# Kernel optimization log

Hardware: AMD Instinct MI355X
Metric: run time of the kernel (lower is better)

Reference implementation:

```python
import jax, jax.numpy as jnp
import numpy as np

N, IN, H0, H1 = 8192, 128, 512, 256
ITER = 10
EPS = 1e-5


def _bn(h, g, b):
    # BatchNorm1d in training mode: biased batch stats
    mu = h.mean(axis=0)
    var = h.var(axis=0)
    return g * (h - mu) * jax.lax.rsqrt(var + EPS) + b


def setup_inputs() -> dict:
    key = jax.random.key(0)
    ks = jax.random.split(key, 8)
    x = jax.random.normal(ks[0], (N, IN), dtype=jnp.float32)
    W = jax.random.uniform(ks[1], (N, N), dtype=jnp.float32)  # torch.rand
    W1 = jax.random.normal(ks[2], (H0, IN), dtype=jnp.float32) * (1.0 / np.sqrt(IN))
    b1 = jnp.zeros((H0,), jnp.float32)
    g1 = jnp.ones((H0,), jnp.float32)
    be1 = jnp.zeros((H0,), jnp.float32)
    W2 = jax.random.normal(ks[3], (H1, H0), dtype=jnp.float32) * (1.0 / np.sqrt(H0))
    b2 = jnp.zeros((H1,), jnp.float32)
    g2 = jnp.ones((H1,), jnp.float32)
    be2 = jnp.zeros((H1,), jnp.float32)
    fcw = jax.random.normal(ks[4], (1, H1), dtype=jnp.float32) * (1.0 / np.sqrt(H1))
    fcb = jnp.zeros((1,), jnp.float32)
    return {"x": x, "W": W, "W1": W1, "b1": b1, "g1": g1, "be1": be1,
            "W2": W2, "b2": b2, "g2": g2, "be2": be2, "fcw": fcw, "fcb": fcb}


def reference(x, W, W1, b1, g1, be1, W2, b2, g2, be2, fcw, fcb):
    h = jax.nn.leaky_relu(_bn(x @ W1.T + b1, g1, be1), 0.01)        # [N, H0]
    feats = jax.nn.leaky_relu(_bn(h @ W2.T + b2, g2, be2), 0.01)    # [N, H1]
    logits = feats @ fcw.T + fcb                                    # [N, 1]
    fn = jnp.linalg.norm(feats, axis=1, keepdims=True)              # [N, 1]
    pairwise_sim = (feats @ feats.T) / (fn @ fn.T)                  # [N, N]
    W_sym = (W + W.T) * 0.5
    PP = pairwise_sim * W_sym                                       # [N, N]
    unary = logits
    def body(i, lg):
        coef = 1.0 - 2.0 * jax.nn.sigmoid(lg)                       # (1-p) - p, [N,1]
        # E_i = sum_j (1-2 p_j) * PP[i, j]  -> matvec
        return unary + PP @ coef
    logits = jax.lax.fori_loop(0, ITER, body, logits)
    return logits
```

## Files before the change

kernel.cpp:

```cpp
#include <hip/hip_runtime.h>
#include <hip/hip_bf16.h>

#define NROWS 8192
#define NITER 10

typedef __attribute__((ext_vector_type(8))) short bf16x8;
typedef __attribute__((ext_vector_type(8))) unsigned short u16x8;
typedef __attribute__((ext_vector_type(16))) float f32x16;

__device__ __forceinline__ float bf2f(unsigned short u) {
  union { float f; unsigned int i; } c; c.i = ((unsigned int)u) << 16; return c.f;
}
__device__ __forceinline__ unsigned short f2bf(float f) {
  unsigned int x = __float_as_uint(f);
  unsigned int r = (x + 0x7FFFu + ((x >> 16) & 1u)) >> 16;
  return (unsigned short)r;
}

#define TRIS(b) ((b) * (257 - (b)) / 2)
__device__ __forceinline__ void tril_decode(int L, int& bi, int& bj) {
  int b = (int)((257.0f - sqrtf((float)(66049 - 8 * L))) * 0.5f);
  if (b > 127) b = 127;
  if (b < 0) b = 0;
  while (b < 127 && TRIS(b + 1) <= L) ++b;
  while (b > 0 && TRIS(b) > L) --b;
  bi = b;
  bj = b + (L - TRIS(b));
}

#define TRIS64(b) ((b) * (129 - (b)) / 2)
__device__ __forceinline__ void tril64_decode(int L, int& bi, int& bj) {
  int b = (int)((129.0f - sqrtf((float)(16641 - 8 * L))) * 0.5f);
  if (b > 63) b = 63;
  if (b < 0) b = 0;
  while (b < 63 && TRIS64(b + 1) <= L) ++b;
  while (b > 0 && TRIS64(b) > L) --b;
  bi = b;
  bj = b + (L - TRIS64(b));
}

__global__ __launch_bounds__(256) void cast3(const float* __restrict__ x,
                                             const float* __restrict__ W1,
                                             const float* __restrict__ W2,
                                             unsigned short* __restrict__ xb,
                                             unsigned short* __restrict__ w1b,
                                             unsigned short* __restrict__ w2b) {
  int idx = blockIdx.x * 256 + threadIdx.x;
  const float* src; unsigned short* dst; int l;
  if (idx < 131072) { src = x; dst = xb; l = idx; }
  else if (idx < 139264) { src = W1; dst = w1b; l = idx - 131072; }
  else if (idx < 155648) { src = W2; dst = w2b; l = idx - 139264; }
  else return;
  const float4* p = (const float4*)src + (size_t)l * 2;
  float4 a = p[0], b = p[1];
  u16x8 o;
  o[0] = f2bf(a.x); o[1] = f2bf(a.y); o[2] = f2bf(a.z); o[3] = f2bf(a.w);
  o[4] = f2bf(b.x); o[5] = f2bf(b.y); o[6] = f2bf(b.z); o[7] = f2bf(b.w);
  *(u16x8*)(dst + (size_t)l * 8) = o;
}

__global__ __launch_bounds__(256) void gemm_bt_mfma_stats(
    const unsigned short* __restrict__ A, const unsigned short* __restrict__ B,
    unsigned short* __restrict__ Cb, float* __restrict__ pS, float* __restrict__ pQ,
    int NN, int K) {
  __shared__ __align__(16) unsigned short Asw[4096];
  __shared__ __align__(16) unsigned short Bsw[4096];
  __shared__ float Sarr[4][64], Qarr[4][64];
  const int i0 = blockIdx.x * 64, j0 = blockIdx.y * 64;
  const int t = threadIdx.x;
  const int lane = t & 63;
  const int wv = t >> 6;
  const int wi = wv >> 1, wj = wv & 1;
  const int khalf = lane >> 5;

  f32x16 acc;
#pragma unroll
  for (int r = 0; r < 16; ++r) acc[r] = 0.f;

  const int lrow = t >> 2;
  const int lgp = (t & 3) * 2;
  const int arow = wi * 32 + (lane & 31);
  const int brow = wj * 32 + (lane & 31);
  const int nc = K >> 6;
#pragma unroll 1
  for (int c = 0; c < nc; ++c) {
    const unsigned short* sa = A + (size_t)(i0 + lrow) * K + c * 64 + lgp * 8;
    const unsigned short* sb = B + (size_t)(j0 + lrow) * K + c * 64 + lgp * 8;
    u16x8 va0 = *(const u16x8*)(sa);
    u16x8 va1 = *(const u16x8*)(sa + 8);
    u16x8 vb0 = *(const u16x8*)(sb);
    u16x8 vb1 = *(const u16x8*)(sb + 8);
    __syncthreads();
    int s0 = (lgp ^ (lrow & 7)) * 8;
    int s1 = ((lgp + 1) ^ (lrow & 7)) * 8;
    *(u16x8*)&Asw[lrow * 64 + s0] = va0;
    *(u16x8*)&Asw[lrow * 64 + s1] = va1;
    *(u16x8*)&Bsw[lrow * 64 + s0] = vb0;
    *(u16x8*)&Bsw[lrow * 64 + s1] = vb1;
    __syncthreads();
#pragma unroll
    for (int s = 0; s < 4; ++s) {
      int slot = s * 2 + khalf;
      bf16x8 a = *(const bf16x8*)&Asw[arow * 64 + ((slot ^ (arow & 7)) * 8)];
      bf16x8 b = *(const bf16x8*)&Bsw[brow * 64 + ((slot ^ (brow & 7)) * 8)];
      acc = __builtin_amdgcn_mfma_f32_32x32x16_bf16(a, b, acc, 0, 0, 0);
    }
  }
  float s = 0.f, q = 0.f;
#pragma unroll
  for (int r = 0; r < 16; ++r) {
    int rowl = (r & 3) + 8 * (r >> 2) + 4 * khalf;
    int coll = lane & 31;
    float v = acc[r];
    s += v; q += v * v;
    Cb[(size_t)(i0 + wi * 32 + rowl) * NN + j0 + wj * 32 + coll] = f2bf(v);
  }
  Sarr[wv][lane] = s;
  Qarr[wv][lane] = q;
  __syncthreads();
  if (t < 64) {
    int wjc = t >> 5, coll = t & 31;
    float st = (Sarr[wjc][coll] + Sarr[wjc][coll + 32]) +
               (Sarr[wjc + 2][coll] + Sarr[wjc + 2][coll + 32]);
    float qt = (Qarr[wjc][coll] + Qarr[wjc][coll + 32]) +
               (Qarr[wjc + 2][coll] + Qarr[wjc + 2][coll + 32]);
    pS[(size_t)blockIdx.x * NN + j0 + t] = st;
    pQ[(size_t)blockIdx.x * NN + j0 + t] = qt;
  }
}

__global__ void bn_finalize(const float* __restrict__ pS, const float* __restrict__ pQ,
                            const float* __restrict__ g, const float* __restrict__ be,
                            float2* __restrict__ ab, int C) {
  int c = blockIdx.x * 256 + threadIdx.x;
  if (c >= C) return;
  float s = 0.f, q = 0.f;
  for (int r = 0; r < 128; ++r) { s += pS[(size_t)r * C + c]; q += pQ[(size_t)r * C + c]; }
  const float invM = 1.f / 8192.f;
  float mu = s * invM;
  float var = q * invM - mu * mu;
  float rstd = rsqrtf(var + 1e-5f);
  float a = g[c] * rstd;
  ab[c] = make_float2(a, be[c] - mu * a);
}

__global__ __launch_bounds__(256) void bn_apply(const unsigned short* __restrict__ hraw,
                                                const float2* __restrict__ ab,
                                                unsigned short* __restrict__ hb,
                                                int Cmask) {
  size_t idx = (size_t)blockIdx.x * 256 + threadIdx.x;
  u16x8 v = *(const u16x8*)(hraw + idx * 8);
  int cb = (int)((idx * 8) & (size_t)Cmask);
  u16x8 o;
#pragma unroll
  for (int k = 0; k < 8; ++k) {
    float2 a = ab[cb + k];
    float r = a.x * bf2f(v[k]) + a.y;
    r = r >= 0.f ? r : 0.01f * r;
    o[k] = f2bf(r);
  }
  *(u16x8*)(hb + idx * 8) = o;
}

__global__ __launch_bounds__(256) void bn_rowfn(const unsigned short* __restrict__ fraw,
                                                const float2* __restrict__ ab,
                                                const float* __restrict__ fcw,
                                                const float* __restrict__ fcb,
                                                unsigned short* __restrict__ fnorm,
                                                float* __restrict__ unary,
                                                float* __restrict__ coef0) {
  const int lane = threadIdx.x & 63;
  const int row = blockIdx.x * 4 + (threadIdx.x >> 6);
  ushort4 v4 = *(const ushort4*)(fraw + (size_t)row * 256 + lane * 4);
  float4 w = *(const float4*)(fcw + lane * 4);
  int c = lane * 4;
  float2 a0 = ab[c], a1 = ab[c + 1], a2 = ab[c + 2], a3 = ab[c + 3];
  float f0 = a0.x * bf2f(v4.x) + a0.y; f0 = f0 >= 0.f ? f0 : 0.01f * f0;
  float f1 = a1.x * bf2f(v4.y) + a1.y; f1 = f1 >= 0.f ? f1 : 0.01f * f1;
  float f2 = a2.x * bf2f(v4.z) + a2.y; f2 = f2 >= 0.f ? f2 : 0.01f * f2;
  float f3 = a3.x * bf2f(v4.w) + a3.y; f3 = f3 >= 0.f ? f3 : 0.01f * f3;
  float ssq = f0 * f0 + f1 * f1 + f2 * f2 + f3 * f3;
  float dot = f0 * w.x + f1 * w.y + f2 * w.z + f3 * w.w;
#pragma unroll
  for (int o = 32; o; o >>= 1) { ssq += __shfl_xor(ssq, o); dot += __shfl_xor(dot, o); }
  float rfn = rsqrtf(ssq);
  *(ushort4*)(fnorm + (size_t)row * 256 + lane * 4) =
      make_ushort4(f2bf(f0 * rfn), f2bf(f1 * rfn), f2bf(f2 * rfn), f2bf(f3 * rfn));
  if (lane == 0) {
    float lg = dot + fcb[0];
    unary[row] = lg;
    coef0[row] = 1.f - 2.f / (1.f + __expf(-lg));
  }
}

__global__ __launch_bounds__(256) void ppbuild_sym(const unsigned short* __restrict__ fnorm,
                                                   const float* __restrict__ W,
                                                   unsigned short* __restrict__ PP) {
  int bi, bj;
  tril_decode(blockIdx.x, bi, bj);
  const int i0 = bi * 64, j0 = bj * 64;

  __shared__ __align__(16) unsigned char shm[18944];
  unsigned short* Asw = (unsigned short*)shm;
  unsigned short* Bsw = (unsigned short*)shm + 4736;
  float (*Wt)[68] = (float(*)[68])shm;
  unsigned short* OutD = (unsigned short*)shm;

  const int t = threadIdx.x;
  const int lane = t & 63;
  const int wv = t >> 6;
  const int wi = wv >> 1, wj = wv & 1;
  const int khalf = lane >> 5;

  f32x16 acc;
#pragma unroll
  for (int r = 0; r < 16; ++r) acc[r] = 0.f;

  const int lrow = t >> 2;
  const int lgp = (t & 3) * 2;
  const int arow = wi * 32 + (lane & 31);
  const int brow = wj * 32 + (lane & 31);
#pragma unroll 1
  for (int c = 0; c < 4; ++c) {
    const unsigned short* sa = fnorm + (size_t)(i0 + lrow) * 256 + c * 64 + lgp * 8;
    const unsigned short* sb = fnorm + (size_t)(j0 + lrow) * 256 + c * 64 + lgp * 8;
    u16x8 va0 = *(const u16x8*)(sa);
    u16x8 va1 = *(const u16x8*)(sa + 8);
    u16x8 vb0 = *(const u16x8*)(sb);
    u16x8 vb1 = *(const u16x8*)(sb + 8);
    __syncthreads();
    int s0 = (lgp ^ (lrow & 7)) * 8;
    int s1 = ((lgp + 1) ^ (lrow & 7)) * 8;
    *(u16x8*)&Asw[lrow * 64 + s0] = va0;
    *(u16x8*)&Asw[lrow * 64 + s1] = va1;
    *(u16x8*)&Bsw[lrow * 64 + s0] = vb0;
    *(u16x8*)&Bsw[lrow * 64 + s1] = vb1;
    __syncthreads();
#pragma unroll
    for (int s = 0; s < 4; ++s) {
      int slot = s * 2 + khalf;
      bf16x8 a = *(const bf16x8*)&Asw[arow * 64 + ((slot ^ (arow & 7)) * 8)];
      bf16x8 b = *(const bf16x8*)&Bsw[brow * 64 + ((slot ^ (brow & 7)) * 8)];
      acc = __builtin_amdgcn_mfma_f32_32x32x16_bf16(a, b, acc, 0, 0, 0);
    }
  }

  __syncthreads();
  {
    const int j = t >> 2, cb = (t & 3) * 16;
    const float* src = W + (size_t)(j0 + j) * NROWS + i0 + cb;
#pragma unroll
    for (int q = 0; q < 4; ++q) {
      float4 v = *(const float4*)(src + q * 4);
      Wt[j][cb + q * 4 + 0] = v.x; Wt[j][cb + q * 4 + 1] = v.y;
      Wt[j][cb + q * 4 + 2] = v.z; Wt[j][cb + q * 4 + 3] = v.w;
    }
  }
  __syncthreads();
  unsigned short pb[16];
#pragma unroll
  for (int r = 0; r < 16; ++r) {
    int rowl = (r & 3) + 8 * (r >> 2) + 4 * khalf;
    int coll = lane & 31;
    int il = wi * 32 + rowl, jl = wj * 32 + coll;
    float wd = W[(size_t)(i0 + il) * NROWS + (j0 + jl)];
    float ws = 0.5f * (wd + Wt[jl][il]);
    pb[r] = f2bf(acc[r] * ws);
  }
  __syncthreads();
#pragma unroll
  for (int r = 0; r < 16; ++r) {
    int rowl = (r & 3) + 8 * (r >> 2) + 4 * khalf;
    int coll = lane & 31;
    OutD[(wi * 32 + rowl) * 74 + wj * 32 + coll] = pb[r];
  }
  __syncthreads();
  const int row = t >> 3;
  const int seg = t & 7;
#pragma unroll
  for (int q = 0; q < 2; ++q) {
    int rr = row + q * 32;
    const unsigned int* pd = (const unsigned int*)(OutD + rr * 74 + seg * 8);
    union { u16x8 v; unsigned int u[4]; } dd;
#pragma unroll
    for (int k = 0; k < 4; ++k) dd.u[k] = pd[k];
    *(u16x8*)(PP + (size_t)(i0 + rr) * NROWS + j0 + seg * 8) = dd.v;
  }
}

__global__ __launch_bounds__(256) void ppmv_sym(const unsigned short* __restrict__ PP,
                                                const float* __restrict__ coef_in,
                                                float* __restrict__ pE) {
  int bi, bj;
  tril64_decode(blockIdx.x, bi, bj);
  const int i0 = bi * 128, j0 = bj * 128;
  const int t = threadIdx.x;

  __shared__ __align__(16) unsigned short tile[128][132];
  __shared__ float cj[128], ci[128];
  __shared__ float Tw[8][128];
  __shared__ float Dred[128];

  if (t < 128) cj[t] = coef_in[j0 + t];
  else ci[t - 128] = coef_in[i0 + (t - 128)];
  {
    const int r = t >> 1, h = (t & 1) * 64;
    const unsigned short* src = PP + (size_t)(i0 + r) * NROWS + j0 + h;
#pragma unroll
    for (int q = 0; q < 8; ++q)
      *(u16x8*)&tile[r][h + q * 8] = *(const u16x8*)(src + q * 8);
  }
  __syncthreads();
  {
    const int r = t >> 1, h = (t & 1) * 64;
    float a = 0.f;
#pragma unroll
    for (int q = 0; q < 8; ++q) {
      u16x8 v = *(const u16x8*)&tile[r][h + q * 8];
      float4 c0 = *(const float4*)&cj[h + q * 8];
      float4 c1 = *(const float4*)&cj[h + q * 8 + 4];
      a += bf2f(v[0]) * c0.x + bf2f(v[1]) * c0.y + bf2f(v[2]) * c0.z + bf2f(v[3]) * c0.w;
      a += bf2f(v[4]) * c1.x + bf2f(v[5]) * c1.y + bf2f(v[6]) * c1.z + bf2f(v[7]) * c1.w;
    }
    a += __shfl_xor(a, 1);
    if ((t & 1) == 0) Dred[r] = a;
  }
  {
    const int c4 = (t & 31) * 4, rg = t >> 5;
    float a0 = 0.f, a1 = 0.f, a2 = 0.f, a3 = 0.f;
#pragma unroll
    for (int k = 0; k < 16; ++k) {
      int row = rg * 16 + k;
      ushort4 v = *(const ushort4*)&tile[row][c4];
      float s = ci[row];
      a0 += bf2f(v.x) * s; a1 += bf2f(v.y) * s;
      a2 += bf2f(v.z) * s; a3 += bf2f(v.w) * s;
    }
    Tw[rg][c4] = a0; Tw[rg][c4 + 1] = a1;
    Tw[rg][c4 + 2] = a2; Tw[rg][c4 + 3] = a3;
  }
  __syncthreads();
  if (t < 128) {
    pE[(size_t)bj * NROWS + i0 + t] = Dred[t];
    if (bi != bj) {
      float s = ((Tw[0][t] + Tw[1][t]) + (Tw[2][t] + Tw[3][t])) +
                ((Tw[4][t] + Tw[5][t]) + (Tw[6][t] + Tw[7][t]));
      pE[(size_t)bi * NROWS + j0 + t] = s;
    }
  }
}

__global__ __launch_bounds__(256) void ppmv_reduce(const float* __restrict__ pE,
                                                   const float* __restrict__ unary,
                                                   float* __restrict__ coef_out,
                                                   float* __restrict__ lg_out) {
  int row = blockIdx.x * 256 + threadIdx.x;
  float acc = 0.f;
#pragma unroll 8
  for (int s = 0; s < 64; ++s) acc += pE[(size_t)s * NROWS + row];
  float lg = unary[row] + acc;
  coef_out[row] = 1.f - 2.f / (1.f + __expf(-lg));
  if (lg_out) lg_out[row] = lg;
}

extern "C" void kernel_launch(void* const* d_in, const int* in_sizes, int n_in,
                              void* d_out, int out_size, void* d_ws, size_t ws_size,
                              hipStream_t stream) {
  const float* x   = (const float*)d_in[0];
  const float* W   = (const float*)d_in[1];
  const float* W1  = (const float*)d_in[2];
  const float* g1  = (const float*)d_in[4];
  const float* be1 = (const float*)d_in[5];
  const float* W2  = (const float*)d_in[6];
  const float* g2  = (const float*)d_in[8];
  const float* be2 = (const float*)d_in[9];
  const float* fcw = (const float*)d_in[10];
  const float* fcb = (const float*)d_in[11];
  float* out = (float*)d_out;

  char* ws = (char*)d_ws;
  unsigned short* hraw = (unsigned short*)(ws + 0);
  float* pE    = (float*)(ws + 0);
  unsigned short* fraw = (unsigned short*)(ws + 8388608);
  float* pS1   = (float*)(ws + 12582912);
  float* pQ1   = (float*)(ws + 12845056);
  float* pS2   = (float*)(ws + 13107200);
  float* pQ2   = (float*)(ws + 13238272);
  float2* ab1  = (float2*)(ws + 13369344);
  float2* ab2  = (float2*)(ws + 13373440);
  unsigned short* fnorm = (unsigned short*)(ws + 13375488);
  float* unary = (float*)(ws + 17569792);
  float* coefA = (float*)(ws + 17602560);
  float* coefB = (float*)(ws + 17635328);
  unsigned short* hb  = (unsigned short*)(ws + 17668096);
  unsigned short* xb  = (unsigned short*)(ws + 26056704);
  unsigned short* w1b = (unsigned short*)(ws + 28153856);
  unsigned short* w2b = (unsigned short*)(ws + 28284928);
  unsigned short* PP  = (unsigned short*)(ws + 28547072);
  if (ws_size < (size_t)162764800) return;

  cast3<<<608, 256, 0, stream>>>(x, W1, W2, xb, w1b, w2b);
  gemm_bt_mfma_stats<<<dim3(128, 8), 256, 0, stream>>>(xb, w1b, hraw, pS1, pQ1, 512, 128);
  bn_finalize<<<2, 256, 0, stream>>>(pS1, pQ1, g1, be1, ab1, 512);
  bn_apply<<<2048, 256, 0, stream>>>(hraw, ab1, hb, 511);
  gemm_bt_mfma_stats<<<dim3(128, 4), 256, 0, stream>>>(hb, w2b, fraw, pS2, pQ2, 256, 512);
  bn_finalize<<<1, 256, 0, stream>>>(pS2, pQ2, g2, be2, ab2, 256);
  bn_rowfn<<<2048, 256, 0, stream>>>(fraw, ab2, fcw, fcb, fnorm, unary, coefA);
  ppbuild_sym<<<8256, 256, 0, stream>>>(fnorm, W, PP);
  float* cur = coefA; float* nxt = coefB;
  for (int it = 0; it < NITER; ++it) {
    ppmv_sym<<<2080, 256, 0, stream>>>(PP, cur, pE);
    ppmv_reduce<<<32, 256, 0, stream>>>(pE, unary, nxt, it == NITER - 1 ? out : nullptr);
    float* tmp = cur; cur = nxt; nxt = tmp;
  }
}
```

Baseline: 326.0 us.

## Fuse first PP matvec iteration into symmetric PP build kernel

The PP build kernel now also computes the first iteration's partial matvec (row and transposed column sums against the initial coefficients) from the bf16 tile it already holds in shared memory. It writes these partials into a 128-slot buffer, which removes one full ppmv_sym pass over the 128 MB PP matrix. The reduce kernel takes a slot count and now runs with 128-thread blocks for more parallelism. The cost is extra shared-memory work and longer tail work in each build block, plus a reduce that sums 128 slots once.

```diff
diff --git a/kernel.cpp b/kernel.cpp
--- a/kernel.cpp
+++ b/kernel.cpp
@@ -195,7 +195,9 @@
 
 __global__ __launch_bounds__(256) void ppbuild_sym(const unsigned short* __restrict__ fnorm,
                                                    const float* __restrict__ W,
-                                                   unsigned short* __restrict__ PP) {
+                                                   unsigned short* __restrict__ PP,
+                                                   const float* __restrict__ coef0,
+                                                   float* __restrict__ pE128) {
   int bi, bj;
   tril_decode(blockIdx.x, bi, bj);
   const int i0 = bi * 64, j0 = bj * 64;
@@ -205,6 +207,10 @@
   unsigned short* Bsw = (unsigned short*)shm + 4736;
   float (*Wt)[68] = (float(*)[68])shm;
   unsigned short* OutD = (unsigned short*)shm;
+  float* cjD = (float*)(shm + 11264);
+  float* ciD = cjD + 64;
+  float* TwD = ciD + 64;
+  float* DrD = TwD + 256;
 
   const int t = threadIdx.x;
   const int lane = t & 63;
@@ -274,17 +280,45 @@
     int coll = lane & 31;
     OutD[(wi * 32 + rowl) * 74 + wj * 32 + coll] = pb[r];
   }
-  __syncthreads();
-  const int row = t >> 3;
-  const int seg = t & 7;
-#pragma unroll
-  for (int q = 0; q < 2; ++q) {
-    int rr = row + q * 32;
-    const unsigned int* pd = (const unsigned int*)(OutD + rr * 74 + seg * 8);
-    union { u16x8 v; unsigned int u[4]; } dd;
-#pragma unroll
-    for (int k = 0; k < 4; ++k) dd.u[k] = pd[k];
-    *(u16x8*)(PP + (size_t)(i0 + rr) * NROWS + j0 + seg * 8) = dd.v;
+  if (t < 64) cjD[t] = coef0[j0 + t];
+  else if (t < 128) ciD[t - 64] = coef0[i0 + (t - 64)];
+  __syncthreads();
+  {
+    const int row = t >> 3;
+    const int seg = t & 7;
+#pragma unroll
+    for (int q = 0; q < 2; ++q) {
+      int rr = row + q * 32;
+      const unsigned int* pd = (const unsigned int*)(OutD + rr * 74 + seg * 8);
+      union { u16x8 v; unsigned int u[4]; } dd;
+#pragma unroll
+      for (int k = 0; k < 4; ++k) dd.u[k] = pd[k];
+      *(u16x8*)(PP + (size_t)(i0 + rr) * NROWS + j0 + seg * 8) = dd.v;
+    }
+  }
+  {
+    int r = t >> 2, c0 = (t & 3) * 16;
+    float a = 0.f;
+#pragma unroll
+    for (int k = 0; k < 16; ++k) a += bf2f(OutD[r * 74 + c0 + k]) * cjD[c0 + k];
+    a += __shfl_xor(a, 1);
+    a += __shfl_xor(a, 2);
+    if ((t & 3) == 0) DrD[r] = a;
+  }
+  {
+    int c = t & 63, w = t >> 6;
+    float a = 0.f;
+#pragma unroll
+    for (int k = 0; k < 16; ++k) a += bf2f(OutD[(w * 16 + k) * 74 + c]) * ciD[w * 16 + k];
+    TwD[w * 64 + c] = a;
+  }
+  __syncthreads();
+  if (t < 64) {
+    pE128[(size_t)bj * NROWS + i0 + t] = DrD[t];
+    if (bi != bj) {
+      float s = (TwD[t] + TwD[64 + t]) + (TwD[128 + t] + TwD[192 + t]);
+      pE128[(size_t)bi * NROWS + j0 + t] = s;
+    }
   }
 }
 
@@ -350,14 +384,15 @@
   }
 }
 
-__global__ __launch_bounds__(256) void ppmv_reduce(const float* __restrict__ pE,
+__global__ __launch_bounds__(128) void ppmv_reduce(const float* __restrict__ pE,
+                                                   int nslots,
                                                    const float* __restrict__ unary,
                                                    float* __restrict__ coef_out,
                                                    float* __restrict__ lg_out) {
-  int row = blockIdx.x * 256 + threadIdx.x;
+  int row = blockIdx.x * 128 + threadIdx.x;
   float acc = 0.f;
 #pragma unroll 8
-  for (int s = 0; s < 64; ++s) acc += pE[(size_t)s * NROWS + row];
+  for (int s = 0; s < nslots; ++s) acc += pE[(size_t)s * NROWS + row];
   float lg = unary[row] + acc;
   coef_out[row] = 1.f - 2.f / (1.f + __expf(-lg));
   if (lg_out) lg_out[row] = lg;
@@ -380,7 +415,8 @@
 
   char* ws = (char*)d_ws;
   unsigned short* hraw = (unsigned short*)(ws + 0);
-  float* pE    = (float*)(ws + 0);
+  float* pE128 = (float*)(ws + 0);
+  float* pE64  = (float*)(ws + 4194304);
   unsigned short* fraw = (unsigned short*)(ws + 8388608);
   float* pS1   = (float*)(ws + 12582912);
   float* pQ1   = (float*)(ws + 12845056);
@@ -406,11 +442,14 @@
   gemm_bt_mfma_stats<<<dim3(128, 4), 256, 0, stream>>>(hb, w2b, fraw, pS2, pQ2, 256, 512);
   bn_finalize<<<1, 256, 0, stream>>>(pS2, pQ2, g2, be2, ab2, 256);
   bn_rowfn<<<2048, 256, 0, stream>>>(fraw, ab2, fcw, fcb, fnorm, unary, coefA);
-  ppbuild_sym<<<8256, 256, 0, stream>>>(fnorm, W, PP);
-  float* cur = coefA; float* nxt = coefB;
-  for (int it = 0; it < NITER; ++it) {
-    ppmv_sym<<<2080, 256, 0, stream>>>(PP, cur, pE);
-    ppmv_reduce<<<32, 256, 0, stream>>>(pE, unary, nxt, it == NITER - 1 ? out : nullptr);
+  ppbuild_sym<<<8256, 256, 0, stream>>>(fnorm, W, PP, coefA, pE128);
+  ppmv_reduce<<<64, 128, 0, stream>>>(pE128, 128, unary, coefB,
+                                      NITER == 1 ? out : nullptr);
+  float* cur = coefB; float* nxt = coefA;
+  for (int it = 2; it <= NITER; ++it) {
+    ppmv_sym<<<2080, 256, 0, stream>>>(PP, cur, pE64);
+    ppmv_reduce<<<64, 128, 0, stream>>>(pE64, 64, unary, nxt,
+                                        it == NITER ? out : nullptr);
     float* tmp = cur; cur = nxt; nxt = tmp;
   }
 }
```

New measurement: 337.4 us. 1.03x slower.
